# Optimization experiments

Hardware: AMD Instinct MI355X
Metric: run time of the kernel (lower is better)

Reference implementation:

```python
import jax, jax.numpy as jnp
import numpy as np

N, E, G = 10000, 40000, 64   # nodes, edges, graphs
ED, H, OUT = 4, 64, 4        # edge_attr_dim, hidden, output_dim


def _nnconv(x, src, dst, edge_attr, w1, b1, w2, b2, root_w, bias, in_dim, out_dim, n_nodes):
    # edge MLP: Linear -> ReLU -> Linear, producing per-edge [in_dim, out_dim] weights
    h = jax.nn.relu(edge_attr @ w1 + b1) @ w2 + b2        # [E, in*out]
    W = h.reshape(-1, in_dim, out_dim)                    # [E, in, out]
    msg = jnp.einsum('ei,eio->eo', x[src], W)             # gather + per-edge matmul
    s = jax.ops.segment_sum(msg, dst, num_segments=n_nodes)
    cnt = jax.ops.segment_sum(jnp.ones((msg.shape[0],), x.dtype), dst, num_segments=n_nodes)
    agg = s / jnp.maximum(cnt, 1.0)[:, None]              # scatter-mean (0 for isolated nodes)
    return agg + x @ root_w + bias                        # NNConv root weight + bias


def setup_inputs():
    key = jax.random.key(0)
    ks = jax.random.split(key, 16)
    lin = lambda k, i, o: jax.random.normal(k, (i, o), jnp.float32) * 0.05
    inp = {}
    inp['node_ids'] = jax.random.normal(ks[0], (N, 1), jnp.float32)
    inp['edge_index'] = jax.random.randint(ks[1], (2, E), 0, N)
    inp['edge_attr'] = jax.random.normal(ks[2], (E, ED), jnp.float32)
    inp['batch'] = jnp.sort(jax.random.randint(ks[3], (N,), 0, G))
    # layer 0: in=1, out=H
    inp['w1_0'] = lin(ks[4], ED, 1 * H); inp['b1_0'] = jnp.zeros((1 * H,), jnp.float32)
    inp['w2_0'] = lin(ks[5], 1 * H, 1 * H); inp['b2_0'] = jnp.zeros((1 * H,), jnp.float32)
    inp['root_0'] = lin(ks[6], 1, H); inp['bias_0'] = jnp.zeros((H,), jnp.float32)
    # layer 1: in=H, out=H
    inp['w1_1'] = lin(ks[7], ED, H * H); inp['b1_1'] = jnp.zeros((H * H,), jnp.float32)
    inp['w2_1'] = lin(ks[8], H * H, H * H); inp['b2_1'] = jnp.zeros((H * H,), jnp.float32)
    inp['root_1'] = lin(ks[9], H, H); inp['bias_1'] = jnp.zeros((H,), jnp.float32)
    # classifier
    inp['wc1'] = lin(ks[10], H, H); inp['bc1'] = jnp.zeros((H,), jnp.float32)
    inp['wc2'] = lin(ks[11], H, OUT); inp['bc2'] = jnp.zeros((OUT,), jnp.float32)
    return inp


def reference(node_ids, edge_index, edge_attr, batch,
              w1_0, b1_0, w2_0, b2_0, root_0, bias_0,
              w1_1, b1_1, w2_1, b2_1, root_1, bias_1,
              wc1, bc1, wc2, bc2):
    src, dst = edge_index[0], edge_index[1]
    x = node_ids
    x = jax.nn.relu(_nnconv(x, src, dst, edge_attr, w1_0, b1_0, w2_0, b2_0, root_0, bias_0, 1, H, N))
    x = jax.nn.relu(_nnconv(x, src, dst, edge_attr, w1_1, b1_1, w2_1, b2_1, root_1, bias_1, H, H, N))
    # dropout omitted (inference mode)
    gs = jax.ops.segment_sum(x, batch, num_segments=G)
    gc = jax.ops.segment_sum(jnp.ones((N,), x.dtype), batch, num_segments=G)
    pooled = gs / jnp.maximum(gc, 1.0)[:, None]           # global_mean_pool
    h = jax.nn.relu(pooled @ wc1 + bc1)
    return h @ wc2 + bc2
```

## Files before the change

kernel.cpp:

```cpp
#include <hip/hip_runtime.h>
#include <hip/hip_fp16.h>

#define N_NODES 10000
#define N_EDGES 40000
#define N_GRAPH 64
#define CPS     258
#define NTILES  1256
#define EPAD    40192
#define PSLICE  (EPAD * 64)

typedef _Float16 half8_t  __attribute__((ext_vector_type(8)));
typedef float    floatx16 __attribute__((ext_vector_type(16)));

__device__ __forceinline__ void gload_lds16(const void* g, void* l) {
  __builtin_amdgcn_global_load_lds((const __attribute__((address_space(1))) void*)g,
                                   (__attribute__((address_space(3))) void*)l, 16, 0, 0);
}

__device__ __host__ __forceinline__ int swz(int row) {
  return ((row & 3) << 1) | ((row >> 2) & 1);
}

__device__ __forceinline__ half8_t splat8(_Float16 v) {
  half8_t r = {v, v, v, v, v, v, v, v};
  return r;
}

union U32H2 { unsigned int u; __half2 h2; };

__global__ void prep_B(const float* __restrict__ w2, const float* __restrict__ b2,
                       _Float16* __restrict__ BC) {
  int tid = blockIdx.x * 256 + threadIdx.x;
  if (tid >= 8 * CPS * 128) return;
  int ks  = tid / (CPS * 128);
  int rem = tid - ks * (CPS * 128);
  int c   = rem >> 7;
  int pos = rem & 127;
  int sl = pos >> 3, j3 = pos & 7;
  _Float16* dstb = BC + ((size_t)(ks * CPS + c) * 64) * 128;
  bool pad = (c > 256) || (c == 256 && ks != 7);
  int kk_l = ks * 32768 + c * 128 + pos;
  int k = kk_l >> 6, i = kk_l & 63;
  if (pad || k > 4096) {
    #pragma unroll 8
    for (int o = 0; o < 64; ++o)
      dstb[o * 128 + ((sl ^ swz(o)) << 3) + j3] = (_Float16)0.f;
  } else if (k < 4096) {
    const float* src = w2 + (size_t)k * 4096 + i * 64;
    #pragma unroll 8
    for (int o = 0; o < 64; ++o)
      dstb[o * 128 + ((sl ^ swz(o)) << 3) + j3] = (_Float16)src[o];
  } else {
    const float* src = b2 + i * 64;
    #pragma unroll 8
    for (int o = 0; o < 64; ++o)
      dstb[o * 128 + ((sl ^ swz(o)) << 3) + j3] = (_Float16)src[o];
  }
}

__global__ void prep_W(const float* __restrict__ w1, const float* __restrict__ b1,
                       unsigned int* __restrict__ WP) {
  int tid = blockIdx.x * 256 + threadIdx.x;
  if (tid >= 8 * 256) return;
  int ks = tid >> 8, c = tid & 255;
  int kb = ks * 512 + 2 * c;
  unsigned int* dst = WP + (size_t)tid * 8;
  #pragma unroll
  for (int d = 0; d < 4; ++d) {
    float2 v = *(const float2*)(w1 + d * 4096 + kb);
    U32H2 u; u.h2 = __floats2half2_rn(v.x, v.y);
    dst[d] = u.u;
  }
  float2 bv = *(const float2*)(b1 + kb);
  U32H2 u; u.h2 = __floats2half2_rn(bv.x, bv.y);
  dst[4] = u.u; dst[5] = 0; dst[6] = 0; dst[7] = 0;
}

__global__ void layer0_edge(const float* __restrict__ node_ids,
                            const int* __restrict__ ei,
                            const float* __restrict__ ea,
                            const float* __restrict__ w1, const float* __restrict__ b1,
                            const float* __restrict__ w2, const float* __restrict__ b2,
                            float* __restrict__ agg0, float* __restrict__ cnt) {
  __shared__ float w1s[256], b1s[64], w2s[4096], b2s[64], zb[4][64];
  int t = threadIdx.x;
  for (int idx = t; idx < 4096; idx += 256) w2s[idx] = w2[idx];
  if (t < 256) w1s[t] = w1[t];
  if (t < 64) { b1s[t] = b1[t]; b2s[t] = b2[t]; }
  __syncthreads();
  int w = t >> 6, l = t & 63;
  int gw = blockIdx.x * 4 + w;
  int nw = gridDim.x * 4;
  for (int e = gw; e < N_EDGES; e += nw) {
    float a0 = ea[e * 4 + 0], a1 = ea[e * 4 + 1], a2 = ea[e * 4 + 2], a3 = ea[e * 4 + 3];
    float z = a0 * w1s[l] + a1 * w1s[64 + l] + a2 * w1s[128 + l] + a3 * w1s[192 + l] + b1s[l];
    zb[w][l] = fmaxf(z, 0.f);
    asm volatile("s_waitcnt lgkmcnt(0)" ::: "memory");
    __builtin_amdgcn_sched_barrier(0);
    float h = b2s[l];
    #pragma unroll
    for (int k = 0; k < 64; ++k) h += zb[w][k] * w2s[k * 64 + l];
    int src = ei[e], dst = ei[N_EDGES + e];
    float msg = node_ids[src] * h;
    atomicAdd(&agg0[dst * 64 + l], msg);
    if (l == 0) atomicAdd(&cnt[dst], 1.0f);
  }
}

__global__ void node0(const float* __restrict__ node_ids, const int* __restrict__ batch,
                      const float* __restrict__ agg0, const float* __restrict__ cnt,
                      const float* __restrict__ root0, const float* __restrict__ bias0,
                      float* __restrict__ x1, float* __restrict__ pcnt) {
  int gid = blockIdx.x * 256 + threadIdx.x;
  if (gid >= N_NODES * 64) return;
  int n = gid >> 6, o = gid & 63;
  float c = fmaxf(cnt[n], 1.f);
  float v = agg0[gid] / c + node_ids[n] * root0[o] + bias0[o];
  x1[gid] = fmaxf(v, 0.f);
  if (o == 0) atomicAdd(&pcnt[batch[n]], 1.0f);
}

template <bool PART>
__launch_bounds__(256, 3)
__global__ void fused_edge_gemm(const int* __restrict__ ei,
                                const float* __restrict__ ea,
                                const float* __restrict__ x1,
                                const unsigned int* __restrict__ WP,
                                const _Float16* __restrict__ BC,
                                float* __restrict__ outbuf) {
  __shared__ __attribute__((aligned(16))) _Float16 Bl[3][64 * 128];
  int t = threadIdx.x;
  int ks = blockIdx.x & 7;
  int eb = blockIdx.x >> 3;
  int e0 = eb * 256;
  int w = t >> 6, l = t & 63;
  int half_ = l >> 5;
  int lane31 = l & 31;
  int swo = swz(lane31);

  half8_t xh8[2][4];
  __half2 eb_bc[2][4];
  #pragma unroll
  for (int m = 0; m < 2; ++m) {
    int e = e0 + w * 64 + m * 32 + lane31;
    if (e < N_EDGES) {
      int src = ei[e];
      const float* xp = x1 + src * 64 + half_ * 8;
      #pragma unroll
      for (int q = 0; q < 4; ++q) {
        float4 f0 = *(const float4*)(xp + q * 16);
        float4 f1 = *(const float4*)(xp + q * 16 + 4);
        half8_t v;
        v[0] = (_Float16)f0.x; v[1] = (_Float16)f0.y;
        v[2] = (_Float16)f0.z; v[3] = (_Float16)f0.w;
        v[4] = (_Float16)f1.x; v[5] = (_Float16)f1.y;
        v[6] = (_Float16)f1.z; v[7] = (_Float16)f1.w;
        xh8[m][q] = v;
      }
      float4 av = *(const float4*)(ea + e * 4);
      eb_bc[m][0] = __float2half2_rn(av.x); eb_bc[m][1] = __float2half2_rn(av.y);
      eb_bc[m][2] = __float2half2_rn(av.z); eb_bc[m][3] = __float2half2_rn(av.w);
    } else {
      #pragma unroll
      for (int q = 0; q < 4; ++q) xh8[m][q] = splat8((_Float16)0.f);
      #pragma unroll
      for (int d = 0; d < 4; ++d) eb_bc[m][d] = __float2half2_rn(0.f);
    }
  }

  floatx16 acc[2][2];
  #pragma unroll
  for (int m = 0; m < 2; ++m)
    #pragma unroll
    for (int n = 0; n < 2; ++n)
      #pragma unroll
      for (int r = 0; r < 16; ++r) acc[m][n][r] = 0.f;

  const char* gp = (const char*)BC + (size_t)ks * (CPS * 16384) + w * 4096 + l * 16;
  char*       sd = (char*)&Bl[0][0] + w * 4096 + l * 16;
  const char* rb = (const char*)&Bl[0][0] + lane31 * 256;
  const unsigned int* wp = WP + (size_t)ks * 256 * 8;

  auto stg = [&](int sb) {
    char* d = sd + sb * 16384;
    gload_lds16(gp,        d);
    gload_lds16(gp + 1024, d + 1024);
    gload_lds16(gp + 2048, d + 2048);
    gload_lds16(gp + 3072, d + 3072);
    gp += 16384;
  };

  const __half zero1 = __float2half(0.f);
  union H2F { __half2 h2; _Float16 f[2]; };
  half8_t zs8[2][2];

  auto zgen = [&](int c) {
    uint4 wv = *(const uint4*)(wp + c * 8);
    unsigned int bb = wp[c * 8 + 4];
    U32H2 uw0, uw1, uw2, uw3, ub;
    uw0.u = wv.x; uw1.u = wv.y; uw2.u = wv.z; uw3.u = wv.w; ub.u = bb;
    #pragma unroll
    for (int m = 0; m < 2; ++m) {
      __half2 h = __hfma2(eb_bc[m][0], uw0.h2, ub.h2);
      h = __hfma2(eb_bc[m][1], uw1.h2, h);
      h = __hfma2(eb_bc[m][2], uw2.h2, h);
      h = __hfma2(eb_bc[m][3], uw3.h2, h);
      H2F u; u.h2 = __halves2half2(__hmax(__low2half(h),  zero1),
                                   __hmax(__high2half(h), zero1));
      zs8[m][0] = splat8(u.f[0]);
      zs8[m][1] = splat8(u.f[1]);
    }
  };
  auto zbias = [&]() {
    #pragma unroll
    for (int m = 0; m < 2; ++m) {
      zs8[m][0] = splat8((_Float16)1.f);
      zs8[m][1] = splat8((_Float16)0.f);
    }
  };

  auto cmp = [&](int rbuf) {
    const char* base = rb + rbuf * 16384;
    __builtin_amdgcn_s_setprio(1);
    #pragma unroll
    for (int t8 = 0; t8 < 8; ++t8) {
      int slot = (t8 * 2 + half_) ^ swo;
      const char* ba = base + slot * 16;
      half8_t bf0 = *(const half8_t*)ba;
      half8_t bf1 = *(const half8_t*)(ba + 8192);
      #pragma unroll
      for (int m = 0; m < 2; ++m) {
        half8_t af = xh8[m][t8 & 3] * zs8[m][t8 >> 2];
        acc[m][0] = __builtin_amdgcn_mfma_f32_32x32x16_f16(af, bf0, acc[m][0], 0, 0, 0);
        acc[m][1] = __builtin_amdgcn_mfma_f32_32x32x16_f16(af, bf1, acc[m][1], 0, 0, 0);
      }
    }
    __builtin_amdgcn_s_setprio(0);
  };

#define SYNC4 do { asm volatile("s_waitcnt vmcnt(4)" ::: "memory"); \
                   __builtin_amdgcn_sched_barrier(0); \
                   __builtin_amdgcn_s_barrier(); \
                   __builtin_amdgcn_sched_barrier(0); } while (0)
#define SYNC0 do { asm volatile("s_waitcnt vmcnt(0)" ::: "memory"); \
                   __builtin_amdgcn_sched_barrier(0); \
                   __builtin_amdgcn_s_barrier(); \
                   __builtin_amdgcn_sched_barrier(0); } while (0)

  stg(0); stg(1);

  int c = 0;
  for (int it = 0; it < 85; ++it) {
    zgen(c);     SYNC4; stg(2); cmp(0);
    zgen(c + 1); SYNC4; stg(0); cmp(1);
    zgen(c + 2); SYNC4; stg(1); cmp(2);
    c += 3;
  }
  zgen(255); SYNC4; stg(2); cmp(0);
  zbias();   SYNC4;         cmp(1);
  zbias();   SYNC0;         cmp(2);

#undef SYNC4
#undef SYNC0

  if (PART) {
    float* pb = outbuf + ((size_t)ks * EPAD + e0 + w * 64) * 64 + lane31;
    #pragma unroll
    for (int m = 0; m < 2; ++m) {
      #pragma unroll
      for (int r = 0; r < 16; ++r) {
        int row = m * 32 + (r & 3) + 8 * (r >> 2) + 4 * half_;
        pb[(size_t)row * 64]      = acc[m][0][r];
        pb[(size_t)row * 64 + 32] = acc[m][1][r];
      }
    }
  } else {
    #pragma unroll
    for (int m = 0; m < 2; ++m) {
      #pragma unroll
      for (int r = 0; r < 16; ++r) {
        int e = e0 + w * 64 + m * 32 + (r & 3) + 8 * (r >> 2) + 4 * half_;
        if (e < N_EDGES) {
          int dst = ei[N_EDGES + e];
          atomicAdd(&outbuf[dst * 64 + lane31],      acc[m][0][r]);
          atomicAdd(&outbuf[dst * 64 + lane31 + 32], acc[m][1][r]);
        }
      }
    }
  }
}

__global__ void reduce_partials(const float* __restrict__ P8, const int* __restrict__ ei,
                                float* __restrict__ agg1) {
  int gid = blockIdx.x * 256 + threadIdx.x;
  if (gid >= N_EDGES * 64) return;
  int e = gid >> 6;
  float s = 0.f;
  #pragma unroll
  for (int ks = 0; ks < 8; ++ks) s += P8[(size_t)ks * PSLICE + gid];
  int dst = ei[N_EDGES + e];
  atomicAdd(&agg1[dst * 64 + (gid & 63)], s);
}

__global__ void node1_pool(const int* __restrict__ batch, const float* __restrict__ x1,
                           const float* __restrict__ agg1, const float* __restrict__ cnt,
                           const float* __restrict__ root1, const float* __restrict__ bias1,
                           float* __restrict__ psum) {
  __shared__ float rt[4096];
  int t = threadIdx.x;
  for (int idx = t; idx < 4096; idx += 256) rt[idx] = root1[idx];
  __syncthreads();
  int w = t >> 6, l = t & 63;
  int n = blockIdx.x * 4 + w;
  if (n >= N_NODES) return;
  float c = fmaxf(cnt[n], 1.f);
  float acc = agg1[n * 64 + l] / c + bias1[l];
  const float* xp = x1 + n * 64;
  #pragma unroll
  for (int i4 = 0; i4 < 16; ++i4) {
    float4 xv = *(const float4*)(xp + i4 * 4);
    acc += xv.x * rt[(i4 * 4 + 0) * 64 + l] + xv.y * rt[(i4 * 4 + 1) * 64 + l]
         + xv.z * rt[(i4 * 4 + 2) * 64 + l] + xv.w * rt[(i4 * 4 + 3) * 64 + l];
  }
  acc = fmaxf(acc, 0.f);
  atomicAdd(&psum[batch[n] * 64 + l], acc);
}

__global__ void classifier(const float* __restrict__ psum, const float* __restrict__ pcnt,
                           const float* __restrict__ wc1, const float* __restrict__ bc1,
                           const float* __restrict__ wc2, const float* __restrict__ bc2,
                           float* __restrict__ out) {
  __shared__ float hb[64];
  int g = blockIdx.x, j = threadIdx.x;
  float c = fmaxf(pcnt[g], 1.f);
  float h = bc1[j];
  const float* pp = psum + g * 64;
  #pragma unroll
  for (int i4 = 0; i4 < 16; ++i4) {
    float4 pv = *(const float4*)(pp + i4 * 4);
    h += (pv.x / c) * wc1[(i4 * 4 + 0) * 64 + j] + (pv.y / c) * wc1[(i4 * 4 + 1) * 64 + j]
       + (pv.z / c) * wc1[(i4 * 4 + 2) * 64 + j] + (pv.w / c) * wc1[(i4 * 4 + 3) * 64 + j];
  }
  hb[j] = fmaxf(h, 0.f);
  __syncthreads();
  if (j < 4) {
    float o = bc2[j];
    #pragma unroll
    for (int k = 0; k < 64; ++k) o += hb[k] * wc2[k * 4 + j];
    out[g * 4 + j] = o;
  }
}

extern "C" void kernel_launch(void* const* d_in, const int* in_sizes, int n_in,
                              void* d_out, int out_size, void* d_ws, size_t ws_size,
                              hipStream_t stream) {
  const float* node_ids = (const float*)d_in[0];
  const int*   ei       = (const int*)d_in[1];
  const float* ea       = (const float*)d_in[2];
  const int*   batch    = (const int*)d_in[3];
  const float* w1_0 = (const float*)d_in[4];
  const float* b1_0 = (const float*)d_in[5];
  const float* w2_0 = (const float*)d_in[6];
  const float* b2_0 = (const float*)d_in[7];
  const float* root0 = (const float*)d_in[8];
  const float* bias0 = (const float*)d_in[9];
  const float* w1_1 = (const float*)d_in[10];
  const float* b1_1 = (const float*)d_in[11];
  const float* w2_1 = (const float*)d_in[12];
  const float* b2_1 = (const float*)d_in[13];
  const float* root1 = (const float*)d_in[14];
  const float* bias1 = (const float*)d_in[15];
  const float* wc1 = (const float*)d_in[16];
  const float* bc1 = (const float*)d_in[17];
  const float* wc2 = (const float*)d_in[18];
  const float* bc2 = (const float*)d_in[19];
  float* out = (float*)d_out;

  char* ws = (char*)d_ws;
  _Float16* BC = (_Float16*)ws;
  unsigned int* WP = (unsigned int*)(ws + 33816576);
  float* x1   = (float*)(ws + 33882112);
  float* agg0 = (float*)(ws + 36442112);
  float* agg1 = (float*)(ws + 39002112);
  float* cnt  = (float*)(ws + 41562112);
  float* psum = (float*)(ws + 41602112);
  float* pcnt = (float*)(ws + 41618496);
  float* P8   = (float*)(ws + 41618752);
  const size_t NEED_PART = 41618752ull + (size_t)8 * PSLICE * 4;

  (void)hipMemsetAsync(agg0, 0, 2560000 + 2560000 + 40000 + 16384 + 256, stream);

  prep_B<<<(8 * CPS * 128 + 255) / 256, 256, 0, stream>>>(w2_1, b2_1, BC);
  prep_W<<<8, 256, 0, stream>>>(w1_1, b1_1, WP);
  layer0_edge<<<512, 256, 0, stream>>>(node_ids, ei, ea, w1_0, b1_0, w2_0, b2_0, agg0, cnt);
  node0<<<(N_NODES * 64 + 255) / 256, 256, 0, stream>>>(node_ids, batch, agg0, cnt, root0, bias0, x1, pcnt);

  if (ws_size >= NEED_PART) {
    fused_edge_gemm<true><<<NTILES, 256, 0, stream>>>(ei, ea, x1, WP, BC, P8);
    reduce_partials<<<(N_EDGES * 64) / 256, 256, 0, stream>>>(P8, ei, agg1);
  } else {
    fused_edge_gemm<false><<<NTILES, 256, 0, stream>>>(ei, ea, x1, WP, BC, agg1);
  }

  node1_pool<<<(N_NODES + 3) / 4, 256, 0, stream>>>(batch, x1, agg1, cnt, root1, bias1, psum);
  classifier<<<N_GRAPH, 64, 0, stream>>>(psum, pcnt, wc1, bc1, wc2, bc2, out);
}
```

Baseline: 1.168 ms.

## Double edges per block in fused edge GEMM to reuse staged B tiles

Measured after the change: 1.222 ms. 1.05x slower.

```diff
diff --git a/kernel.cpp b/kernel.cpp
--- a/kernel.cpp
+++ b/kernel.cpp
@@ -5,8 +5,8 @@
 #define N_EDGES 40000
 #define N_GRAPH 64
 #define CPS     258
-#define NTILES  1256
-#define EPAD    40192
+#define NTILES  632
+#define EPAD    40448
 #define PSLICE  (EPAD * 64)
 
 typedef _Float16 half8_t  __attribute__((ext_vector_type(8)));
@@ -19,11 +19,6 @@
 
 __device__ __host__ __forceinline__ int swz(int row) {
   return ((row & 3) << 1) | ((row >> 2) & 1);
-}
-
-__device__ __forceinline__ half8_t splat8(_Float16 v) {
-  half8_t r = {v, v, v, v, v, v, v, v};
-  return r;
 }
 
 union U32H2 { unsigned int u; __half2 h2; };
@@ -121,7 +116,7 @@
 }
 
 template <bool PART>
-__launch_bounds__(256, 3)
+__launch_bounds__(256, 2)
 __global__ void fused_edge_gemm(const int* __restrict__ ei,
                                 const float* __restrict__ ea,
                                 const float* __restrict__ x1,
@@ -132,17 +127,17 @@
   int t = threadIdx.x;
   int ks = blockIdx.x & 7;
   int eb = blockIdx.x >> 3;
-  int e0 = eb * 256;
+  int e0 = eb * 512;
   int w = t >> 6, l = t & 63;
   int half_ = l >> 5;
   int lane31 = l & 31;
   int swo = swz(lane31);
 
-  half8_t xh8[2][4];
-  __half2 eb_bc[2][4];
-  #pragma unroll
-  for (int m = 0; m < 2; ++m) {
-    int e = e0 + w * 64 + m * 32 + lane31;
+  __half2 xh2[4][4][4];
+  __half2 eb_bc[4][4];
+  #pragma unroll
+  for (int m = 0; m < 4; ++m) {
+    int e = e0 + w * 128 + m * 32 + lane31;
     if (e < N_EDGES) {
       int src = ei[e];
       const float* xp = x1 + src * 64 + half_ * 8;
@@ -150,27 +145,27 @@
       for (int q = 0; q < 4; ++q) {
         float4 f0 = *(const float4*)(xp + q * 16);
         float4 f1 = *(const float4*)(xp + q * 16 + 4);
-        half8_t v;
-        v[0] = (_Float16)f0.x; v[1] = (_Float16)f0.y;
-        v[2] = (_Float16)f0.z; v[3] = (_Float16)f0.w;
-        v[4] = (_Float16)f1.x; v[5] = (_Float16)f1.y;
-        v[6] = (_Float16)f1.z; v[7] = (_Float16)f1.w;
-        xh8[m][q] = v;
+        xh2[m][q][0] = __floats2half2_rn(f0.x, f0.y);
+        xh2[m][q][1] = __floats2half2_rn(f0.z, f0.w);
+        xh2[m][q][2] = __floats2half2_rn(f1.x, f1.y);
+        xh2[m][q][3] = __floats2half2_rn(f1.z, f1.w);
       }
       float4 av = *(const float4*)(ea + e * 4);
       eb_bc[m][0] = __float2half2_rn(av.x); eb_bc[m][1] = __float2half2_rn(av.y);
       eb_bc[m][2] = __float2half2_rn(av.z); eb_bc[m][3] = __float2half2_rn(av.w);
     } else {
       #pragma unroll
-      for (int q = 0; q < 4; ++q) xh8[m][q] = splat8((_Float16)0.f);
+      for (int q = 0; q < 4; ++q)
+        #pragma unroll
+        for (int p = 0; p < 4; ++p) xh2[m][q][p] = __floats2half2_rn(0.f, 0.f);
       #pragma unroll
       for (int d = 0; d < 4; ++d) eb_bc[m][d] = __float2half2_rn(0.f);
     }
   }
 
-  floatx16 acc[2][2];
-  #pragma unroll
-  for (int m = 0; m < 2; ++m)
+  floatx16 acc[4][2];
+  #pragma unroll
+  for (int m = 0; m < 4; ++m)
     #pragma unroll
     for (int n = 0; n < 2; ++n)
       #pragma unroll
@@ -191,8 +186,7 @@
   };
 
   const __half zero1 = __float2half(0.f);
-  union H2F { __half2 h2; _Float16 f[2]; };
-  half8_t zs8[2][2];
+  __half2 z2[4][2];
 
   auto zgen = [&](int c) {
     uint4 wv = *(const uint4*)(wp + c * 8);
@@ -200,22 +194,20 @@
     U32H2 uw0, uw1, uw2, uw3, ub;
     uw0.u = wv.x; uw1.u = wv.y; uw2.u = wv.z; uw3.u = wv.w; ub.u = bb;
     #pragma unroll
-    for (int m = 0; m < 2; ++m) {
+    for (int m = 0; m < 4; ++m) {
       __half2 h = __hfma2(eb_bc[m][0], uw0.h2, ub.h2);
       h = __hfma2(eb_bc[m][1], uw1.h2, h);
       h = __hfma2(eb_bc[m][2], uw2.h2, h);
       h = __hfma2(eb_bc[m][3], uw3.h2, h);
-      H2F u; u.h2 = __halves2half2(__hmax(__low2half(h),  zero1),
-                                   __hmax(__high2half(h), zero1));
-      zs8[m][0] = splat8(u.f[0]);
-      zs8[m][1] = splat8(u.f[1]);
+      z2[m][0] = __half2half2(__hmax(__low2half(h),  zero1));
+      z2[m][1] = __half2half2(__hmax(__high2half(h), zero1));
     }
   };
   auto zbias = [&]() {
     #pragma unroll
-    for (int m = 0; m < 2; ++m) {
-      zs8[m][0] = splat8((_Float16)1.f);
-      zs8[m][1] = splat8((_Float16)0.f);
+    for (int m = 0; m < 4; ++m) {
+      z2[m][0] = __floats2half2_rn(1.f, 1.f);
+      z2[m][1] = __floats2half2_rn(0.f, 0.f);
     }
   };
 
@@ -229,10 +221,12 @@
       half8_t bf0 = *(const half8_t*)ba;
       half8_t bf1 = *(const half8_t*)(ba + 8192);
       #pragma unroll
-      for (int m = 0; m < 2; ++m) {
-        half8_t af = xh8[m][t8 & 3] * zs8[m][t8 >> 2];
-        acc[m][0] = __builtin_amdgcn_mfma_f32_32x32x16_f16(af, bf0, acc[m][0], 0, 0, 0);
-        acc[m][1] = __builtin_amdgcn_mfma_f32_32x32x16_f16(af, bf1, acc[m][1], 0, 0, 0);
+      for (int m = 0; m < 4; ++m) {
+        union { half8_t v; __half2 p[4]; } af;
+        #pragma unroll
+        for (int p = 0; p < 4; ++p) af.p[p] = __hmul2(xh2[m][t8 & 3][p], z2[m][t8 >> 2]);
+        acc[m][0] = __builtin_amdgcn_mfma_f32_32x32x16_f16(af.v, bf0, acc[m][0], 0, 0, 0);
+        acc[m][1] = __builtin_amdgcn_mfma_f32_32x32x16_f16(af.v, bf1, acc[m][1], 0, 0, 0);
       }
     }
     __builtin_amdgcn_s_setprio(0);
@@ -264,9 +258,9 @@
 #undef SYNC0
 
   if (PART) {
-    float* pb = outbuf + ((size_t)ks * EPAD + e0 + w * 64) * 64 + lane31;
-    #pragma unroll
-    for (int m = 0; m < 2; ++m) {
+    float* pb = outbuf + ((size_t)ks * EPAD + e0 + w * 128) * 64 + lane31;
+    #pragma unroll
+    for (int m = 0; m < 4; ++m) {
       #pragma unroll
       for (int r = 0; r < 16; ++r) {
         int row = m * 32 + (r & 3) + 8 * (r >> 2) + 4 * half_;
@@ -276,10 +270,10 @@
     }
   } else {
     #pragma unroll
-    for (int m = 0; m < 2; ++m) {
+    for (int m = 0; m < 4; ++m) {
       #pragma unroll
       for (int r = 0; r < 16; ++r) {
-        int e = e0 + w * 64 + m * 32 + (r & 3) + 8 * (r >> 2) + 4 * half_;
+        int e = e0 + w * 128 + m * 32 + (r & 3) + 8 * (r >> 2) + 4 * half_;
         if (e < N_EDGES) {
           int dst = ei[N_EDGES + e];
           atomicAdd(&outbuf[dst * 64 + lane31],      acc[m][0][r]);
@@ -397,7 +391,7 @@
 
   if (ws_size >= NEED_PART) {
     fused_edge_gemm<true><<<NTILES, 256, 0, stream>>>(ei, ea, x1, WP, BC, P8);
-    reduce_partials<<<(N_EDGES * 64) / 256, 256, 0, stream>>>(P8, ei, agg1);
+    reduce_partials<<<(N_EDGES * 64 + 255) / 256, 256, 0, stream>>>(P8, ei, agg1);
   } else {
     fused_edge_gemm<false><<<NTILES, 256, 0, stream>>>(ei, ea, x1, WP, BC, agg1);
   }
```
